# Kernel optimization log

Measured on AMD Instinct MI355X. Metric: run time of the kernel, lower is better.

## Reference

```python
import jax, jax.numpy as jnp
import numpy as np

EPS = 1e-06


def setup_inputs() -> dict:
    key = jax.random.key(0)
    ks = jax.random.split(key, 8)
    B, T, D = 4, 1024, 1024  # module requires T == D (diagonal einsum)
    s = 1.0 / np.sqrt(D)
    return {
        "x_seq": jax.random.normal(ks[0], (B, T, D), dtype=jnp.float32),
        "gamma": jnp.asarray(0.9, dtype=jnp.float32),
        "Wq": jax.random.normal(ks[1], (D, D), dtype=jnp.float32) * s,
        "bq": jax.random.normal(ks[2], (D,), dtype=jnp.float32) * 0.01,
        "Wk": jax.random.normal(ks[3], (D, D), dtype=jnp.float32) * s,
        "bk": jax.random.normal(ks[4], (D,), dtype=jnp.float32) * 0.01,
        "Wv": jax.random.normal(ks[5], (D, D), dtype=jnp.float32) * s,
        "bv": jax.random.normal(ks[6], (D,), dtype=jnp.float32) * 0.01,
    }


def reference(x_seq, gamma, Wq, bq, Wk, bk, Wv, bv):
    # Faithful math of SUPRAParallelFixedGamma.forward. Notes on fidelity:
    # - torch einsum 'ij,bjdj->bidj' takes the DIAGONAL of kv over (time, last
    #   v-dim), i.e. kv[b,j,d,j] = k[b,j,d] * v[b,j,j]; requires T == D.
    # - gamma_exponents = arange(T)[None,:] - arange(T)[:,None] -> E[i,j] = max(j-i, 0)
    #   (the clamp leaves PAST entries at gamma**0 == 1 and decays FUTURE ones).
    # - S = cumsum over dim 1 (the 'i'/time-output axis) then contracted with q;
    #   this factors exactly as C = cumsum(G, axis=0) applied as a (T,T) weight,
    #   avoiding the original's O(B*T*D*T) intermediate while computing the same math.
    B, T, D = x_seq.shape
    q = jax.nn.relu(x_seq @ Wq.T + bq)          # phi(W_q x)
    k = jax.nn.relu(x_seq @ Wk.T + bk)          # phi(W_k x)
    v = x_seq @ Wv.T + bv
    t = jnp.arange(T)
    E = jnp.maximum(t[None, :] - t[:, None], 0).astype(x_seq.dtype)  # (T,T)
    G = gamma ** E                               # gamma_powers[i,j] = gamma**max(j-i,0)
    C = jnp.cumsum(G, axis=0)                    # C[t,j] = sum_{t'<=t} G[t',j]
    vd = jnp.diagonal(v, axis1=1, axis2=2)       # (B,T): v[b,j,j]  (T==D)
    kv_diag = k * vd[:, :, None]                 # (B,T,D): kv[b,j,d,j]
    # num[b,t,j] = sum_d q[b,t,d] * C[t,j] * kv_diag[b,j,d]
    num = C[None, :, :] * jnp.einsum('btd,bjd->btj', q, kv_diag)
    # Z[b,t,d] = cumsum_t of (G @ k) = sum_j C[t,j] k[b,j,d]
    Z = jnp.einsum('tj,bjd->btd', C, k)
    denom = jnp.sum(q * Z, axis=-1, keepdims=True) + EPS
    return num / denom
```

## Files before the change

### kernel.cpp

```cpp
#include <hip/hip_runtime.h>

typedef __attribute__((ext_vector_type(8))) short bf16x8;
typedef __attribute__((ext_vector_type(4))) float f32x4;


__device__ __forceinline__ unsigned short f2bf(float f) {
    unsigned int u = __builtin_bit_cast(unsigned int, f);
    u += 0x7fffu + ((u >> 16) & 1u);
    return (unsigned short)(u >> 16);
}

__device__ __forceinline__ float bf2f(unsigned short s) {
    return __builtin_bit_cast(float, (unsigned int)s << 16);
}

__device__ __forceinline__ void g2lds16(const unsigned short* g, unsigned short* l) {
    __builtin_amdgcn_global_load_lds(
        (const __attribute__((address_space(1))) unsigned int*)g,
        (__attribute__((address_space(3))) unsigned int*)l, 16, 0, 0);
}


__global__ __launch_bounds__(256)
void pack3_kernel(const float* __restrict__ x, const float* __restrict__ wq,
                  const float* __restrict__ wk, unsigned short* __restrict__ xb,
                  unsigned short* __restrict__ wqk, int n4x, int n4w) {
    int i = blockIdx.x * 256 + threadIdx.x;
    const float* src; unsigned short* dst; int idx;
    if (i < n4x)            { src = x;  dst = xb;  idx = i; }
    else if (i < n4x + n4w) { src = wq; dst = wqk; idx = i - n4x; }
    else                    { src = wk; dst = wqk + (size_t)n4w * 4; idx = i - n4x - n4w; }
    float4 v = reinterpret_cast<const float4*>(src)[idx];
    union { unsigned short s[4]; uint2 u; } o;
    o.s[0] = f2bf(v.x); o.s[1] = f2bf(v.y); o.s[2] = f2bf(v.z); o.s[3] = f2bf(v.w);
    reinterpret_cast<uint2*>(dst)[idx] = o.u;
}


__global__ __launch_bounds__(256)
void vdiag_kernel(const unsigned short* __restrict__ xb, const float* __restrict__ Wv,
                  const float* __restrict__ bv, float* __restrict__ vd) {
    int w = blockIdx.x * 4 + (threadIdx.x >> 6);
    int lane = threadIdx.x & 63;
    int b = w >> 10, j = w & 1023;
    const unsigned short* xr = xb + (size_t)(b * 1024 + j) * 1024;
    const float* wr = Wv + (size_t)j * 1024;
    float s = 0.f;
    #pragma unroll
    for (int e = 0; e < 2; ++e) {
        int base = e * 512 + lane * 8;
        bf16x8 xv = *reinterpret_cast<const bf16x8*>(xr + base);
        float4 w0 = *reinterpret_cast<const float4*>(wr + base);
        float4 w1 = *reinterpret_cast<const float4*>(wr + base + 4);
        s = fmaf(bf2f((unsigned short)xv[0]), w0.x, s);
        s = fmaf(bf2f((unsigned short)xv[1]), w0.y, s);
        s = fmaf(bf2f((unsigned short)xv[2]), w0.z, s);
        s = fmaf(bf2f((unsigned short)xv[3]), w0.w, s);
        s = fmaf(bf2f((unsigned short)xv[4]), w1.x, s);
        s = fmaf(bf2f((unsigned short)xv[5]), w1.y, s);
        s = fmaf(bf2f((unsigned short)xv[6]), w1.z, s);
        s = fmaf(bf2f((unsigned short)xv[7]), w1.w, s);
    }
    #pragma unroll
    for (int off = 32; off; off >>= 1) s += __shfl_down(s, off, 64);
    if (lane == 0) vd[w] = s + bv[j];
}


template<int MODE>
__global__ __launch_bounds__(256, 2)
void gemm_kernel(const unsigned short* __restrict__ A, const unsigned short* __restrict__ Bm,
                 unsigned short* __restrict__ qb, unsigned short* __restrict__ kb,
                 const float* __restrict__ bq, const float* __restrict__ bk,
                 unsigned short* __restrict__ nmb, const float* __restrict__ vd,
                 float* __restrict__ dpart, const float* __restrict__ gammap,
                 int K, int Mtot) {
    __shared__ unsigned short lA[2][128 * 32];
    __shared__ unsigned short lB[2][128 * 32];

    const int tid = threadIdx.x;
    const int lane = tid & 63;
    const int wid = tid >> 6;
    const int wr = wid >> 1, wc = wid & 1;
    const int tileM = blockIdx.y * 128, tileN = blockIdx.x * 128;

    const long bsAB = (MODE == 1) ? (long)1024 * 1024 : 0;
    const unsigned short* Ab = A + blockIdx.z * bsAB;
    const unsigned short* Bb = Bm + blockIdx.z * bsAB;

    const int r0 = tid >> 2;
    const int r1 = (tid + 256) >> 2;
    const int cc = (tid & 3) * 8;
    const int frow = lane & 15;
    const int fk = (lane >> 4) * 8;

    f32x4 acc[4][4];
    #pragma unroll
    for (int m = 0; m < 4; ++m)
        #pragma unroll
        for (int n = 0; n < 4; ++n)
            acc[m][n] = (f32x4){0.f, 0.f, 0.f, 0.f};

    auto stage = [&](int buf, int k0) {
        g2lds16(Ab + (size_t)(tileM + r0) * K + (k0 + cc), &lA[buf][tid * 8]);
        g2lds16(Ab + (size_t)(tileM + r1) * K + (k0 + cc), &lA[buf][2048 + tid * 8]);
        g2lds16(Bb + (size_t)(tileN + r0) * K + (k0 + cc), &lB[buf][tid * 8]);
        g2lds16(Bb + (size_t)(tileN + r1) * K + (k0 + cc), &lB[buf][2048 + tid * 8]);
    };

    stage(0, 0);
    __syncthreads();
    int cur = 0;
    for (int k0 = 0; k0 < K; k0 += 32) {
        if (k0 + 32 < K) stage(cur ^ 1, k0 + 32);

        bf16x8 af[4], bfr[4];
        #pragma unroll
        for (int m = 0; m < 4; ++m)
            af[m] = *reinterpret_cast<const bf16x8*>(&lA[cur][(wr * 64 + m * 16 + frow) * 32 + fk]);
        #pragma unroll
        for (int n = 0; n < 4; ++n)
            bfr[n] = *reinterpret_cast<const bf16x8*>(&lB[cur][(wc * 64 + n * 16 + frow) * 32 + fk]);

        #pragma unroll
        for (int m = 0; m < 4; ++m)
            #pragma unroll
            for (int n = 0; n < 4; ++n)
                acc[m][n] = __builtin_amdgcn_mfma_f32_16x16x32_bf16(af[m], bfr[n], acc[m][n], 0, 0, 0);

        __syncthreads();
        cur ^= 1;
    }

    const int orow = (lane >> 4) * 4;
    const int ocol = lane & 15;

    if constexpr (MODE == 0) {
        const bool isQ = tileN < 1024;
        unsigned short* Cq = isQ ? qb : kb;
        const float* bias = isQ ? bq : bk;
        const int cb = tileN - (isQ ? 0 : 1024);
        #pragma unroll
        for (int n = 0; n < 4; ++n) {
            int col = cb + wc * 64 + n * 16 + ocol;
            float bia = bias[col];
            #pragma unroll
            for (int m = 0; m < 4; ++m) {
                #pragma unroll
                for (int i = 0; i < 4; ++i) {
                    int row = tileM + wr * 64 + m * 16 + orow + i;
                    float v = acc[m][n][i] + bia;
                    Cq[(size_t)row * 1024 + col] = f2bf(v > 0.f ? v : 0.f);
                }
            }
        }
    } else {
        unsigned short* ob = nmb + (size_t)blockIdx.z * 1024 * 1024;
        const float* vdb = vd + blockIdx.z * 1024;
        const float g = gammap[0];
        const float l2g = log2f(g);
        const float inv1mg = 1.f / (1.f - g);
        const float c1 = g * inv1mg;

        int jcol[4]; float gj[4], vdv[4];
        #pragma unroll
        for (int n = 0; n < 4; ++n) {
            jcol[n] = tileN + wc * 64 + n * 16 + ocol;
            gj[n] = exp2f((float)jcol[n] * l2g);
            vdv[n] = vdb[jcol[n]];
        }

        #pragma unroll
        for (int m = 0; m < 4; ++m) {
            #pragma unroll
            for (int i = 0; i < 4; ++i) {
                int t = tileM + wr * 64 + m * 16 + orow + i;
                float gt = exp2f((float)t * l2g);
                float ctf = (1.f - g * gt) * inv1mg;
                float s = 0.f;
                #pragma unroll
                for (int n = 0; n < 4; ++n) {
                    int j = jcol[n];
                    float Cfut = exp2f((float)(j - t) * l2g) * ctf;
                    float Cpast = (float)(t - j + 1) + c1 * (1.f - gj[n]);
                    float Cw = (j <= t) ? Cpast : Cfut;
                    float v = acc[m][n][i];
                    s += Cw * v;
                    ob[(size_t)t * 1024 + j] = f2bf(Cw * vdv[n] * v);
                }
                s += __shfl_xor(s, 1, 64);
                s += __shfl_xor(s, 2, 64);
                s += __shfl_xor(s, 4, 64);
                s += __shfl_xor(s, 8, 64);
                if ((lane & 15) == 0)
                    dpart[(size_t)(blockIdx.x * 2 + wc) * Mtot + blockIdx.z * 1024 + t] = s;
            }
        }
    }
}


__global__ __launch_bounds__(256)
void scale_kernel(const unsigned short* __restrict__ nmb, float* __restrict__ out,
                  const float* __restrict__ dpart, int Mtot) {
    int r = blockIdx.x;
    float s = 1e-6f;
    #pragma unroll
    for (int p = 0; p < 16; ++p) s += dpart[(size_t)p * Mtot + r];
    float inv = 1.f / s;
    const uint2* src = reinterpret_cast<const uint2*>(nmb + (size_t)r * 1024);
    float4* dst = reinterpret_cast<float4*>(out + (size_t)r * 1024);
    uint2 u = src[threadIdx.x];
    float4 v = { bf2f((unsigned short)(u.x & 0xffff)) * inv,
                 bf2f((unsigned short)(u.x >> 16))    * inv,
                 bf2f((unsigned short)(u.y & 0xffff)) * inv,
                 bf2f((unsigned short)(u.y >> 16))    * inv };
    dst[threadIdx.x] = v;
}


extern "C" void kernel_launch(void* const* d_in, const int* in_sizes, int n_in,
                              void* d_out, int out_size, void* d_ws, size_t ws_size,
                              hipStream_t stream) {
    const float* x     = (const float*)d_in[0];
    const float* gamma = (const float*)d_in[1];
    const float* Wq    = (const float*)d_in[2];
    const float* bq    = (const float*)d_in[3];
    const float* Wk    = (const float*)d_in[4];
    const float* bk    = (const float*)d_in[5];
    const float* Wv    = (const float*)d_in[6];
    const float* bv    = (const float*)d_in[7];
    float* out = (float*)d_out;

    const int D = 1024, T = 1024;
    const int B = in_sizes[0] / (T * D);
    const int M = B * T;

    char* ws = (char*)d_ws;
    size_t off = 0;
    unsigned short* xb  = (unsigned short*)(ws + off); off += (size_t)M * D * 2;
    unsigned short* wqk = (unsigned short*)(ws + off); off += (size_t)2 * D * D * 2;
    unsigned short* qb  = (unsigned short*)(ws + off); off += (size_t)M * D * 2;
    unsigned short* kb  = (unsigned short*)(ws + off); off += (size_t)M * D * 2;
    float* vd    = (float*)(ws + off); off += (size_t)M * 4;
    float* dpart = (float*)(ws + off); off += (size_t)16 * M * 4;
    unsigned short* nmb = xb;

    const int n4x = M * D / 4, n4w = D * D / 4;

    pack3_kernel<<<dim3((n4x + 2 * n4w) / 256), 256, 0, stream>>>(x, Wq, Wk, xb, wqk, n4x, n4w);

    vdiag_kernel<<<dim3(M / 4), 256, 0, stream>>>(xb, Wv, bv, vd);

    gemm_kernel<0><<<dim3(2048 / 128, M / 128, 1), 256, 0, stream>>>(
        xb, wqk, qb, kb, bq, bk, nullptr, nullptr, nullptr, nullptr, D, M);

    gemm_kernel<1><<<dim3(T / 128, T / 128, B), 256, 0, stream>>>(
        qb, kb, nullptr, nullptr, nullptr, nullptr, nmb, vd, dpart, gamma, D, M);

    scale_kernel<<<dim3(M), 256, 0, stream>>>(nmb, out, dpart, M);
}
```

Baseline: 79.64 us.

## Fuse denominator scaling into attention GEMM epilogue via inter-block stripe barrier

Removes the separate scale kernel and the bf16 intermediate numerator buffer. Each MODE-1 GEMM block keeps its scaled numerator in registers, publishes its partial denominators, and waits on an atomic counter until all 8 blocks in its row stripe have done the same. It then reads the full denominator sums and writes fp32 output directly. This saves a kernel launch and a write-then-read round trip of the numerator, at the cost of a spin barrier. That barrier assumes all 256 blocks are co-resident and could deadlock otherwise; it also holds registers while blocks wait.

After: 89.84 us. +12.8%, slower.

```diff
diff --git a/kernel.cpp b/kernel.cpp
--- a/kernel.cpp
+++ b/kernel.cpp
@@ -24,8 +24,10 @@
 __global__ __launch_bounds__(256)
 void pack3_kernel(const float* __restrict__ x, const float* __restrict__ wq,
                   const float* __restrict__ wk, unsigned short* __restrict__ xb,
-                  unsigned short* __restrict__ wqk, int n4x, int n4w) {
+                  unsigned short* __restrict__ wqk, int* __restrict__ ready,
+                  int n4x, int n4w) {
     int i = blockIdx.x * 256 + threadIdx.x;
+    if (blockIdx.x == 0 && threadIdx.x < 64) ready[threadIdx.x] = 0;
     const float* src; unsigned short* dst; int idx;
     if (i < n4x)            { src = x;  dst = xb;  idx = i; }
     else if (i < n4x + n4w) { src = wq; dst = wqk; idx = i - n4x; }
@@ -72,9 +74,9 @@
 void gemm_kernel(const unsigned short* __restrict__ A, const unsigned short* __restrict__ Bm,
                  unsigned short* __restrict__ qb, unsigned short* __restrict__ kb,
                  const float* __restrict__ bq, const float* __restrict__ bk,
-                 unsigned short* __restrict__ nmb, const float* __restrict__ vd,
-                 float* __restrict__ dpart, const float* __restrict__ gammap,
-                 int K, int Mtot) {
+                 float* __restrict__ out, const float* __restrict__ vd,
+                 float* __restrict__ dpart, int* __restrict__ ready,
+                 const float* __restrict__ gammap, int K, int Mtot) {
     __shared__ unsigned short lA[2][128 * 32];
     __shared__ unsigned short lB[2][128 * 32];
 
@@ -155,7 +157,7 @@
             }
         }
     } else {
-        unsigned short* ob = nmb + (size_t)blockIdx.z * 1024 * 1024;
+        float* ob = out + (size_t)blockIdx.z * 1024 * 1024;
         const float* vdb = vd + blockIdx.z * 1024;
         const float g = gammap[0];
         const float l2g = log2f(g);
@@ -186,7 +188,7 @@
                     float Cw = (j <= t) ? Cpast : Cfut;
                     float v = acc[m][n][i];
                     s += Cw * v;
-                    ob[(size_t)t * 1024 + j] = f2bf(Cw * vdv[n] * v);
+                    acc[m][n][i] = Cw * vdv[n] * v;
                 }
                 s += __shfl_xor(s, 1, 64);
                 s += __shfl_xor(s, 2, 64);
@@ -196,26 +198,42 @@
                     dpart[(size_t)(blockIdx.x * 2 + wc) * Mtot + blockIdx.z * 1024 + t] = s;
             }
         }
+
+        const int stripe = blockIdx.z * 8 + blockIdx.y;
+        __syncthreads();
+        if (tid == 0) {
+            __threadfence();
+            atomicAdd(&ready[stripe], 1);
+            while (__hip_atomic_load(&ready[stripe], __ATOMIC_ACQUIRE,
+                                     __HIP_MEMORY_SCOPE_AGENT) < 8)
+                __builtin_amdgcn_s_sleep(1);
+            __threadfence();
+        }
+        __syncthreads();
+
+        float* inv_s = reinterpret_cast<float*>(lA);
+        if (tid < 128) {
+            float dsum = 1e-6f;
+            #pragma unroll
+            for (int p = 0; p < 16; ++p)
+                dsum += dpart[(size_t)p * Mtot + blockIdx.z * 1024 + tileM + tid];
+            inv_s[tid] = 1.f / dsum;
+        }
+        __syncthreads();
+
+        #pragma unroll
+        for (int m = 0; m < 4; ++m) {
+            #pragma unroll
+            for (int i = 0; i < 4; ++i) {
+                int tl = wr * 64 + m * 16 + orow + i;
+                float inv = inv_s[tl];
+                size_t rowoff = (size_t)(tileM + tl) * 1024;
+                #pragma unroll
+                for (int n = 0; n < 4; ++n)
+                    ob[rowoff + jcol[n]] = acc[m][n][i] * inv;
+            }
+        }
     }
-}
-
-
-__global__ __launch_bounds__(256)
-void scale_kernel(const unsigned short* __restrict__ nmb, float* __restrict__ out,
-                  const float* __restrict__ dpart, int Mtot) {
-    int r = blockIdx.x;
-    float s = 1e-6f;
-    #pragma unroll
-    for (int p = 0; p < 16; ++p) s += dpart[(size_t)p * Mtot + r];
-    float inv = 1.f / s;
-    const uint2* src = reinterpret_cast<const uint2*>(nmb + (size_t)r * 1024);
-    float4* dst = reinterpret_cast<float4*>(out + (size_t)r * 1024);
-    uint2 u = src[threadIdx.x];
-    float4 v = { bf2f((unsigned short)(u.x & 0xffff)) * inv,
-                 bf2f((unsigned short)(u.x >> 16))    * inv,
-                 bf2f((unsigned short)(u.y & 0xffff)) * inv,
-                 bf2f((unsigned short)(u.y >> 16))    * inv };
-    dst[threadIdx.x] = v;
 }
 
 
@@ -244,19 +262,18 @@
     unsigned short* kb  = (unsigned short*)(ws + off); off += (size_t)M * D * 2;
     float* vd    = (float*)(ws + off); off += (size_t)M * 4;
     float* dpart = (float*)(ws + off); off += (size_t)16 * M * 4;
-    unsigned short* nmb = xb;
+    int* ready   = (int*)(ws + off);   off += 64 * 4;
 
     const int n4x = M * D / 4, n4w = D * D / 4;
 
-    pack3_kernel<<<dim3((n4x + 2 * n4w) / 256), 256, 0, stream>>>(x, Wq, Wk, xb, wqk, n4x, n4w);
+    pack3_kernel<<<dim3((n4x + 2 * n4w) / 256), 256, 0, stream>>>(
+        x, Wq, Wk, xb, wqk, ready, n4x, n4w);
 
     vdiag_kernel<<<dim3(M / 4), 256, 0, stream>>>(xb, Wv, bv, vd);
 
     gemm_kernel<0><<<dim3(2048 / 128, M / 128, 1), 256, 0, stream>>>(
-        xb, wqk, qb, kb, bq, bk, nullptr, nullptr, nullptr, nullptr, D, M);
+        xb, wqk, qb, kb, bq, bk, nullptr, nullptr, nullptr, nullptr, nullptr, D, M);
 
     gemm_kernel<1><<<dim3(T / 128, T / 128, B), 256, 0, stream>>>(
-        qb, kb, nullptr, nullptr, nullptr, nullptr, nmb, vd, dpart, gamma, D, M);
-
-    scale_kernel<<<dim3(M), 256, 0, stream>>>(nmb, out, dpart, M);
-}
+        qb, kb, nullptr, nullptr, nullptr, nullptr, out, vd, dpart, ready, gamma, D, M);
+}
```
